# Performance work log

Hardware: AMD Instinct MI355X
Metric: run time of the kernel (lower is better)

Reference implementation:

```python
import jax, jax.numpy as jnp
import numpy as np

PI = float(np.pi)
TWO_PI = 2.0 * PI
LOG_2PI = float(np.log(TWO_PI))
N_FFT = 1024
LOG_N = 10
N_MAX = min(N_FFT, 2000)  # evaluate_z term cap


def _bitrev_indices(N, num_bits):
    idx = np.arange(N)
    rev = np.zeros(N, dtype=np.int32)
    v = idx.copy()
    for _ in range(num_bits):
        rev = (rev << 1) | (v & 1)
        v >>= 1
    return rev

_BITREV = jnp.asarray(_bitrev_indices(N_FFT, LOG_N))


def fft_fused(x_re, x_im):
    """Radix-2 DIT FFT with bit-reversal load, mirroring the Triton kernel.
    x_re/x_im: [B, N]. Returns (y_re, y_im)."""
    B, N = x_re.shape
    y = (x_re + 1j * x_im).astype(jnp.complex64)[:, _BITREV]
    for stage in range(LOG_N):
        s = 1 << stage          # half butterfly size (stride)
        # twiddles W_k = exp(-2*pi*i*k/(2s)), k in [0, s)
        k = jnp.arange(s)
        w = jnp.exp((-TWO_PI * 1j / (2 * s)) * k).astype(jnp.complex64)
        yg = y.reshape(B, N // (2 * s), 2, s)
        upper = yg[:, :, 0, :]
        lower = yg[:, :, 1, :] * w  # broadcast over [B, groups, s]
        y = jnp.concatenate([upper + lower, upper - lower], axis=-1).reshape(B, N)
    return jnp.real(y), jnp.imag(y)


def evaluate_z(t):
    """Riemann-Siegel Z(t) cosine sum with dynamic term count, masked."""
    t_half = t * 0.5
    theta = t_half * (jnp.log(t) - LOG_2PI) - t_half - PI / 8.0
    theta = theta + 1.0 / (48.0 * t)
    n = jnp.arange(1, N_MAX + 1, dtype=t.dtype)
    log_n = jnp.log(n)
    rsqrt_n = jax.lax.rsqrt(n)
    # [P, N_MAX] outer product of phases
    phases = t[:, None] * log_n[None, :] - theta[:, None]
    terms = rsqrt_n[None, :] * jnp.cos(phases)
    n_terms = jnp.clip(jnp.sqrt(jax.lax.stop_gradient(t) / TWO_PI).astype(jnp.int32), 10, N_MAX)
    mask = jnp.arange(N_MAX)[None, :] < n_terms[:, None]
    return 2.0 * jnp.sum(jnp.where(mask, terms, 0.0), axis=-1)


def setup_inputs() -> dict:
    key = jax.random.key(0)
    k1, k2, k3 = jax.random.split(key, 3)
    x_re = jax.random.normal(k1, (16384, N_FFT), dtype=jnp.float32)
    x_im = jax.random.normal(k2, (16384, N_FFT), dtype=jnp.float32)
    # evaluation points t in [1000, 101000)
    t = 1000.0 + 100000.0 * jax.random.uniform(k3, (262144,), dtype=jnp.float32)
    return {"x_re": x_re, "x_im": x_im, "t": t}


def reference(x_re, x_im, t):
    y_re, y_im = fft_fused(x_re, x_im)
    Z = evaluate_z(t)
    return (y_re, y_im, Z)
```

## Files before the change

### kernel.cpp

```cpp
#include <hip/hip_runtime.h>
#include <math.h>

#define INV_2PI_D 0.15915494309189535

__device__ __forceinline__ void wrev(float rev, float& c, float& s) {
    s = __builtin_amdgcn_sinf(rev);
    c = __builtin_amdgcn_cosf(rev);
}

template<int S>
__device__ __forceinline__ float xshfl(float x) {
    if constexpr (S == 1)
        return __int_as_float(__builtin_amdgcn_mov_dpp(__float_as_int(x), 0xB1, 0xF, 0xF, true));
    else if constexpr (S == 2)
        return __int_as_float(__builtin_amdgcn_mov_dpp(__float_as_int(x), 0x4E, 0xF, 0xF, true));
    else if constexpr (S == 8)
        return __int_as_float(__builtin_amdgcn_mov_dpp(__float_as_int(x), 0x128, 0xF, 0xF, true));
    else if constexpr (S == 4)
        return __int_as_float(__builtin_amdgcn_ds_swizzle(__float_as_int(x), 0x101F));
    else if constexpr (S == 16)
        return __int_as_float(__builtin_amdgcn_ds_swizzle(__float_as_int(x), 0x401F));
    else
        return __shfl_xor(x, 32, 64);
}

template<int S>
__device__ __forceinline__ void stage_x(float (&re)[16], float (&im)[16], int lane) {
    float wr, wi;
    wrev(-(float)(lane & (S - 1)) * (0.5f / (float)S), wr, wi);
    const bool up = (lane & S) == 0;
    const float c1r = up ? 1.0f : -wr;
    const float c1i = up ? 0.0f : -wi;
    const float c2r = up ? wr : 1.0f;
    const float c2i = up ? wi : 0.0f;
#pragma unroll
    for (int r = 0; r < 16; ++r) {
        const float pr = xshfl<S>(re[r]);
        const float pi = xshfl<S>(im[r]);
        const float a = re[r], b = im[r];
        re[r] = a * c1r - b * c1i + pr * c2r - pi * c2i;
        im[r] = a * c1i + b * c1r + pr * c2i + pi * c2r;
    }
}

__device__ __forceinline__ void stage_x1(float (&re)[16], float (&im)[16], int lane) {
    const float sgn = (lane & 1) ? -1.0f : 1.0f;
#pragma unroll
    for (int r = 0; r < 16; ++r) {
        const float pr = xshfl<1>(re[r]);
        const float pi = xshfl<1>(im[r]);
        re[r] = __fmaf_rn(sgn, re[r], pr);
        im[r] = __fmaf_rn(sgn, im[r], pi);
    }
}

__device__ __forceinline__ void bfly(float& ar, float& ai, float& br, float& bi,
                                     float wr, float wi) {
    const float tr = wr * br - wi * bi;
    const float ti = wr * bi + wi * br;
    br = ar - tr; bi = ai - ti;
    ar = ar + tr; ai = ai + ti;
}

template<int M>
__device__ __forceinline__ void stage_r(float (&re)[16], float (&im)[16], float lanef) {
    float cw[M], sw[M];
#pragma unroll
    for (int m = 0; m < M; ++m)
        wrev(-(64.0f * (float)m + lanef) * (1.0f / (128.0f * (float)M)), cw[m], sw[m]);
#pragma unroll
    for (int rl = 0; rl < 16; ++rl) {
        if (rl & M) continue;
        bfly(re[rl], im[rl], re[rl | M], im[rl | M], cw[rl & (M - 1)], sw[rl & (M - 1)]);
    }
}

__device__ __forceinline__ void fft_row(
    const float* __restrict__ xre, const float* __restrict__ xim,
    float* __restrict__ yre, float* __restrict__ yim, int row)
{
    const int lane = (int)(threadIdx.x & 63u);
    const size_t base = (size_t)row << 10;

    float re[16], im[16];

    const int rev6l = (int)(__brev((unsigned)lane) >> 26);
    const float4* xr4 = reinterpret_cast<const float4*>(xre + base) + (rev6l << 2);
    const float4* xi4 = reinterpret_cast<const float4*>(xim + base) + (rev6l << 2);

    static constexpr int RM[4][4] = {
        {0, 8, 4, 12}, {2, 10, 6, 14}, {1, 9, 5, 13}, {3, 11, 7, 15}};
#pragma unroll
    for (int q = 0; q < 4; ++q) {
        const float4 vr = xr4[q];
        const float4 vi = xi4[q];
        re[RM[q][0]] = vr.x; re[RM[q][1]] = vr.y; re[RM[q][2]] = vr.z; re[RM[q][3]] = vr.w;
        im[RM[q][0]] = vi.x; im[RM[q][1]] = vi.y; im[RM[q][2]] = vi.z; im[RM[q][3]] = vi.w;
    }

    stage_x1(re, im, lane);
    stage_x<2>(re, im, lane);
    stage_x<4>(re, im, lane);
    stage_x<8>(re, im, lane);
    stage_x<16>(re, im, lane);
    stage_x<32>(re, im, lane);

    const float lanef = (float)lane;
    stage_r<1>(re, im, lanef);
    stage_r<2>(re, im, lanef);
    stage_r<4>(re, im, lanef);
    stage_r<8>(re, im, lanef);

    float* yr = yre + base + lane;
    float* yi = yim + base + lane;
#pragma unroll
    for (int r = 0; r < 16; ++r) {
        yr[r << 6] = re[r];
        yi[r << 6] = im[r];
    }
}

__global__ __launch_bounds__(256) void table_kernel(float* __restrict__ ws) {
    const int i = (int)(blockIdx.x * 256 + threadIdx.x);
    if (i < 1024) {
        const double nd = (double)(i + 1);
        ws[i]        = (float)log(nd);
        ws[1024 + i] = (float)(1.0 / sqrt(nd));
    }
}

__device__ void z_eval(const float* __restrict__ tin, float* __restrict__ zout,
                       const float* __restrict__ ws, int zblock, int n,
                       float* __restrict__ buf)
{
    for (int i = (int)threadIdx.x; i < 512; i += 256)
        reinterpret_cast<float4*>(buf)[i] = reinterpret_cast<const float4*>(ws)[i];
    __syncthreads();
    const float* slog = buf;
    const float* srsq = buf + 1024;

    const int gid = zblock * 256 + (int)threadIdx.x;
    if (gid >= n) return;

    const float t  = tin[gid];
    const float th = __fmul_rn(t, 0.5f);
    const float logt = (float)log((double)t);
    float theta = __fsub_rn(__fsub_rn(__fmul_rn(th, __fsub_rn(logt, 1.8378770664093453f)), th),
                            0.39269908169872414f);
    theta = __fadd_rn(theta, __fdiv_rn(1.0f, __fmul_rn(48.0f, t)));

    int nt = (int)sqrtf(__fdiv_rn(t, 6.283185307179586f));
    nt = min(max(nt, 10), 1024);

    float acc = 0.0f;
    for (int i = 0; i < nt; ++i) {
        const float p = __fsub_rn(__fmul_rn(t, slog[i]), theta);
        const double rev = (double)p * INV_2PI_D;
        const double fr  = rev - rint(rev);
        const float  c   = __builtin_amdgcn_cosf((float)fr);
        acc = __fmaf_rn(srsq[i], c, acc);
    }
    zout[gid] = __fmul_rn(2.0f, acc);
}

__global__ __launch_bounds__(256, 4) void fused_kernel(
    const float* __restrict__ xre, const float* __restrict__ xim,
    const float* __restrict__ tin, const float* __restrict__ ws,
    float* __restrict__ yre, float* __restrict__ yim, float* __restrict__ zout,
    int z_blocks, int nrows, int nz)
{
    __shared__ float zbuf[2048];

    const int b = (int)blockIdx.x;
    if (b < z_blocks) {
        z_eval(tin, zout, ws, b, nz, zbuf);
    } else {
        const int wid = (int)(threadIdx.x >> 6);
        const int row = ((b - z_blocks) << 2) | wid;
        if (row < nrows)
            fft_row(xre, xim, yre, yim, row);
    }
}

extern "C" void kernel_launch(void* const* d_in, const int* in_sizes, int n_in,
                              void* d_out, int out_size, void* d_ws, size_t ws_size,
                              hipStream_t stream)
{
    const float* xre = (const float*)d_in[0];
    const float* xim = (const float*)d_in[1];
    const float* t   = (const float*)d_in[2];

    const size_t nfft = (size_t)in_sizes[0];
    const int nrows = (int)(nfft >> 10);
    const int nz    = in_sizes[2];

    float* yre = (float*)d_out;
    float* yim = yre + nfft;
    float* z   = yre + 2 * nfft;
    float* ws  = (float*)d_ws;

    table_kernel<<<4, 256, 0, stream>>>(ws);

    const int f_blocks = (nrows + 3) >> 2;
    const int z_blocks = (nz + 255) >> 8;
    fused_kernel<<<z_blocks + f_blocks, 256, 0, stream>>>(
        xre, xim, t, ws, yre, yim, z, z_blocks, nrows, nz);
}
```

Before: 58.64 us.

## Pipeline four FFT rows per wave, inline table build, batch shuffles

```diff
diff --git a/kernel.cpp b/kernel.cpp
--- a/kernel.cpp
+++ b/kernel.cpp
@@ -26,6 +26,9 @@
 
 template<int S>
 __device__ __forceinline__ void stage_x(float (&re)[16], float (&im)[16], int lane) {
+    float pr[16], pi[16];
+#pragma unroll
+    for (int r = 0; r < 16; ++r) { pr[r] = xshfl<S>(re[r]); pi[r] = xshfl<S>(im[r]); }
     float wr, wi;
     wrev(-(float)(lane & (S - 1)) * (0.5f / (float)S), wr, wi);
     const bool up = (lane & S) == 0;
@@ -35,22 +38,21 @@
     const float c2i = up ? wi : 0.0f;
 #pragma unroll
     for (int r = 0; r < 16; ++r) {
-        const float pr = xshfl<S>(re[r]);
-        const float pi = xshfl<S>(im[r]);
         const float a = re[r], b = im[r];
-        re[r] = a * c1r - b * c1i + pr * c2r - pi * c2i;
-        im[r] = a * c1i + b * c1r + pr * c2i + pi * c2r;
+        re[r] = a * c1r - b * c1i + pr[r] * c2r - pi[r] * c2i;
+        im[r] = a * c1i + b * c1r + pr[r] * c2i + pi[r] * c2r;
     }
 }
 
 __device__ __forceinline__ void stage_x1(float (&re)[16], float (&im)[16], int lane) {
+    float pr[16], pi[16];
+#pragma unroll
+    for (int r = 0; r < 16; ++r) { pr[r] = xshfl<1>(re[r]); pi[r] = xshfl<1>(im[r]); }
     const float sgn = (lane & 1) ? -1.0f : 1.0f;
 #pragma unroll
     for (int r = 0; r < 16; ++r) {
-        const float pr = xshfl<1>(re[r]);
-        const float pi = xshfl<1>(im[r]);
-        re[r] = __fmaf_rn(sgn, re[r], pr);
-        im[r] = __fmaf_rn(sgn, im[r], pi);
+        re[r] = __fmaf_rn(sgn, re[r], pr[r]);
+        im[r] = __fmaf_rn(sgn, im[r], pi[r]);
     }
 }
 
@@ -75,42 +77,43 @@
     }
 }
 
-__device__ __forceinline__ void fft_row(
+static constexpr int RM_[4][4] = {
+    {0, 8, 4, 12}, {2, 10, 6, 14}, {1, 9, 5, 13}, {3, 11, 7, 15}};
+
+__device__ __forceinline__ void load_row(
     const float* __restrict__ xre, const float* __restrict__ xim,
-    float* __restrict__ yre, float* __restrict__ yim, int row)
-{
-    const int lane = (int)(threadIdx.x & 63u);
-    const size_t base = (size_t)row << 10;
-
-    float re[16], im[16];
-
-    const int rev6l = (int)(__brev((unsigned)lane) >> 26);
+    size_t base, int rev6l, float (&re)[16], float (&im)[16])
+{
     const float4* xr4 = reinterpret_cast<const float4*>(xre + base) + (rev6l << 2);
     const float4* xi4 = reinterpret_cast<const float4*>(xim + base) + (rev6l << 2);
-
-    static constexpr int RM[4][4] = {
-        {0, 8, 4, 12}, {2, 10, 6, 14}, {1, 9, 5, 13}, {3, 11, 7, 15}};
 #pragma unroll
     for (int q = 0; q < 4; ++q) {
         const float4 vr = xr4[q];
         const float4 vi = xi4[q];
-        re[RM[q][0]] = vr.x; re[RM[q][1]] = vr.y; re[RM[q][2]] = vr.z; re[RM[q][3]] = vr.w;
-        im[RM[q][0]] = vi.x; im[RM[q][1]] = vi.y; im[RM[q][2]] = vi.z; im[RM[q][3]] = vi.w;
-    }
-
+        re[RM_[q][0]] = vr.x; re[RM_[q][1]] = vr.y; re[RM_[q][2]] = vr.z; re[RM_[q][3]] = vr.w;
+        im[RM_[q][0]] = vi.x; im[RM_[q][1]] = vi.y; im[RM_[q][2]] = vi.z; im[RM_[q][3]] = vi.w;
+    }
+}
+
+__device__ __forceinline__ void fft_compute(float (&re)[16], float (&im)[16],
+                                            int lane, float lanef)
+{
     stage_x1(re, im, lane);
     stage_x<2>(re, im, lane);
     stage_x<4>(re, im, lane);
     stage_x<8>(re, im, lane);
     stage_x<16>(re, im, lane);
     stage_x<32>(re, im, lane);
-
-    const float lanef = (float)lane;
     stage_r<1>(re, im, lanef);
     stage_r<2>(re, im, lanef);
     stage_r<4>(re, im, lanef);
     stage_r<8>(re, im, lanef);
-
+}
+
+__device__ __forceinline__ void store_row(
+    float* __restrict__ yre, float* __restrict__ yim,
+    size_t base, int lane, float (&re)[16], float (&im)[16])
+{
     float* yr = yre + base + lane;
     float* yi = yim + base + lane;
 #pragma unroll
@@ -120,24 +123,48 @@
     }
 }
 
-__global__ __launch_bounds__(256) void table_kernel(float* __restrict__ ws) {
-    const int i = (int)(blockIdx.x * 256 + threadIdx.x);
-    if (i < 1024) {
+__device__ void fft_wave(const float* __restrict__ xre, const float* __restrict__ xim,
+                         float* __restrict__ yre, float* __restrict__ yim, int row0)
+{
+    const int lane = (int)(threadIdx.x & 63u);
+    const float lanef = (float)lane;
+    const int rev6l = (int)(__brev((unsigned)lane) >> 26);
+
+    const size_t b0 = (size_t)row0 << 10;
+    const size_t b1 = (size_t)(row0 + 1) << 10;
+    const size_t b2 = (size_t)(row0 + 2) << 10;
+    const size_t b3 = (size_t)(row0 + 3) << 10;
+
+    float Ar[16], Ai[16], Br[16], Bi[16];
+
+    load_row(xre, xim, b0, rev6l, Ar, Ai);
+    load_row(xre, xim, b1, rev6l, Br, Bi);
+    fft_compute(Ar, Ai, lane, lanef);
+    store_row(yre, yim, b0, lane, Ar, Ai);
+
+    load_row(xre, xim, b2, rev6l, Ar, Ai);
+    fft_compute(Br, Bi, lane, lanef);
+    store_row(yre, yim, b1, lane, Br, Bi);
+
+    load_row(xre, xim, b3, rev6l, Br, Bi);
+    fft_compute(Ar, Ai, lane, lanef);
+    store_row(yre, yim, b2, lane, Ar, Ai);
+
+    fft_compute(Br, Bi, lane, lanef);
+    store_row(yre, yim, b3, lane, Br, Bi);
+}
+
+__device__ void z_eval(const float* __restrict__ tin, float* __restrict__ zout,
+                       int zblock, int n, float* __restrict__ buf)
+{
+    float* slog = buf;
+    float* srsq = buf + 1024;
+    for (int i = (int)threadIdx.x; i < 1024; i += 256) {
         const double nd = (double)(i + 1);
-        ws[i]        = (float)log(nd);
-        ws[1024 + i] = (float)(1.0 / sqrt(nd));
-    }
-}
-
-__device__ void z_eval(const float* __restrict__ tin, float* __restrict__ zout,
-                       const float* __restrict__ ws, int zblock, int n,
-                       float* __restrict__ buf)
-{
-    for (int i = (int)threadIdx.x; i < 512; i += 256)
-        reinterpret_cast<float4*>(buf)[i] = reinterpret_cast<const float4*>(ws)[i];
+        slog[i] = (float)log(nd);
+        srsq[i] = (float)(1.0 / sqrt(nd));
+    }
     __syncthreads();
-    const float* slog = buf;
-    const float* srsq = buf + 1024;
 
     const int gid = zblock * 256 + (int)threadIdx.x;
     if (gid >= n) return;
@@ -165,7 +192,7 @@
 
 __global__ __launch_bounds__(256, 4) void fused_kernel(
     const float* __restrict__ xre, const float* __restrict__ xim,
-    const float* __restrict__ tin, const float* __restrict__ ws,
+    const float* __restrict__ tin,
     float* __restrict__ yre, float* __restrict__ yim, float* __restrict__ zout,
     int z_blocks, int nrows, int nz)
 {
@@ -173,12 +200,12 @@
 
     const int b = (int)blockIdx.x;
     if (b < z_blocks) {
-        z_eval(tin, zout, ws, b, nz, zbuf);
+        z_eval(tin, zout, b, nz, zbuf);
     } else {
         const int wid = (int)(threadIdx.x >> 6);
-        const int row = ((b - z_blocks) << 2) | wid;
-        if (row < nrows)
-            fft_row(xre, xim, yre, yim, row);
+        const int row0 = ((b - z_blocks) << 4) + (wid << 2);
+        if (row0 + 3 < nrows)
+            fft_wave(xre, xim, yre, yim, row0);
     }
 }
 
@@ -197,12 +224,9 @@
     float* yre = (float*)d_out;
     float* yim = yre + nfft;
     float* z   = yre + 2 * nfft;
-    float* ws  = (float*)d_ws;
-
-    table_kernel<<<4, 256, 0, stream>>>(ws);
-
-    const int f_blocks = (nrows + 3) >> 2;
+
+    const int f_blocks = (nrows + 15) >> 4;
     const int z_blocks = (nz + 255) >> 8;
     fused_kernel<<<z_blocks + f_blocks, 256, 0, stream>>>(
-        xre, xim, t, ws, yre, yim, z, z_blocks, nrows, nz);
-}
+        xre, xim, t, yre, yim, z, z_blocks, nrows, nz);
+}
```

New measurement: 69.42 us. +18.4%, slower.
